# Kernel tuning notes

Measured on AMD Instinct MI355X. Metric: run time of the kernel, lower is better.

## Reference

```python
import jax, jax.numpy as jnp
import numpy as np
from jax import lax

L = 15      # time_conv_size
STRIDE = 2


def setup_inputs() -> dict:
    key = jax.random.key(0)
    k1, k2, k3 = jax.random.split(key, 3)
    x = jax.random.normal(k1, (8, 4096, 64), dtype=jnp.float32)
    w1 = jax.random.normal(k2, (L,), dtype=jnp.float32)
    w2 = jax.random.normal(k3, (L,), dtype=jnp.float32)
    return {"x": x, "w1": w1, "w2": w2}


def reference(x, w1, w2):
    # x: [B, T, C]; w1, w2: [L]
    B, T, C = x.shape
    p = L // 2
    # --- weighted local mean: mu[b,t,c] = sum_k w1[k] * x_pad[b,t+k,c] ---
    x_pad = jnp.pad(x, ((0, 0), (p, p), (0, 0)))
    mu = sum(w1[k] * x_pad[:, k:k + T, :] for k in range(L))  # [B,T,C]
    # --- centered diagonal bilinear (covariance) pooling ---
    xc_pad = jnp.pad(x - mu, ((0, 0), (p, p), (0, 0)))  # [B, T+2p, C]
    # strided window indices: I = ceil(T/STRIDE) windows of length L
    starts = jnp.arange(0, T, STRIDE)                   # [I]
    idx = starts[:, None] + jnp.arange(L)[None, :]      # [I, L]
    win = xc_pad[:, idx, :]                             # [B, I, L, C]
    sigma = jnp.einsum('bilc,l,bild->bicd', win, w2, win)
    I = starts.shape[0]
    sigma = sigma.reshape(B, I, C * C)
    mu_s = mu[:, ::STRIDE, :]                           # [B, I, C]
    out = jnp.concatenate([mu_s, sigma], axis=-1)       # [B, I, C + C*C]
    # K.l2_normalize over last axis (epsilon=1e-12)
    denom = lax.rsqrt(jnp.maximum(jnp.sum(out * out, axis=-1, keepdims=True), 1e-12))
    return out * denom
```

## Files before the change

kernel.cpp:

```cpp
#include <hip/hip_runtime.h>

#define Tdim 4096
#define Bdim 8
#define Cdim 64
#define Ldim 15
#define Idim 2048
#define OUTW 4160

__global__ __launch_bounds__(256) void cbp_kernel(const float* __restrict__ x,
                                                  const float* __restrict__ w1,
                                                  const float* __restrict__ w2,
                                                  float* __restrict__ out) {
    __shared__ float xbuf[29][64];
    __shared__ float xcs[15][64];
    __shared__ float mus[64];
    __shared__ float w1s[16], w2s[16];
    __shared__ float red[4];
    __shared__ float scale_s;

    const int tid = threadIdx.x;
    const int blk = blockIdx.x;
    const int b = blk >> 11;
    const int i = blk & (Idim - 1);
    const int s = i << 1;

    if (tid < Ldim) { w1s[tid] = w1[tid]; w2s[tid] = w2[tid]; }

    const float* xb = x + (size_t)b * Tdim * Cdim;
    for (int v = tid; v < 29 * 16; v += 256) {
        const int r = v >> 4;
        const int c4 = (v & 15) << 2;
        const int t = s - 14 + r;
        float4 val = make_float4(0.f, 0.f, 0.f, 0.f);
        if (t >= 0 && t < Tdim) val = *(const float4*)(xb + (size_t)t * Cdim + c4);
        *(float4*)(&xbuf[r][c4]) = val;
    }
    __syncthreads();

    if (tid < 240) {
        const int l = tid >> 4;
        const int c4 = (tid & 15) << 2;
        const int t = s - 7 + l;
        float4 m = make_float4(0.f, 0.f, 0.f, 0.f);
#pragma unroll
        for (int k = 0; k < Ldim; ++k) {
            const float w = w1s[k];
            const float4 xv = *(const float4*)(&xbuf[l + k][c4]);
            m.x = fmaf(w, xv.x, m.x);
            m.y = fmaf(w, xv.y, m.y);
            m.z = fmaf(w, xv.z, m.z);
            m.w = fmaf(w, xv.w, m.w);
        }
        const float4 xv = *(const float4*)(&xbuf[l + 7][c4]);
        float4 xc;
        if (t >= 0 && t < Tdim) {
            xc = make_float4(xv.x - m.x, xv.y - m.y, xv.z - m.z, xv.w - m.w);
        } else {
            xc = make_float4(0.f, 0.f, 0.f, 0.f);
        }
        *(float4*)(&xcs[l][c4]) = xc;
        if (l == 7) *(float4*)(&mus[c4]) = m;
    }
    __syncthreads();

    const int q  = tid >> 4;
    const int d0 = (tid & 15) << 2;
    float acc[4][4];
#pragma unroll
    for (int jj = 0; jj < 4; ++jj)
#pragma unroll
        for (int dd = 0; dd < 4; ++dd) acc[jj][dd] = 0.f;

#pragma unroll
    for (int l = 0; l < Ldim; ++l) {
        const float4 xd = *(const float4*)(&xcs[l][d0]);
        const float w = w2s[l];
#pragma unroll
        for (int jj = 0; jj < 4; ++jj) {
            const float a = w * xcs[l][jj * 16 + q];
            acc[jj][0] = fmaf(a, xd.x, acc[jj][0]);
            acc[jj][1] = fmaf(a, xd.y, acc[jj][1]);
            acc[jj][2] = fmaf(a, xd.z, acc[jj][2]);
            acc[jj][3] = fmaf(a, xd.w, acc[jj][3]);
        }
    }

    float local = 0.f;
#pragma unroll
    for (int jj = 0; jj < 4; ++jj)
#pragma unroll
        for (int dd = 0; dd < 4; ++dd) local = fmaf(acc[jj][dd], acc[jj][dd], local);
    if (tid < Cdim) local = fmaf(mus[tid], mus[tid], local);

#pragma unroll
    for (int off = 32; off; off >>= 1) local += __shfl_down(local, off, 64);
    if ((tid & 63) == 0) red[tid >> 6] = local;
    __syncthreads();
    if (tid == 0) {
        const float ss = red[0] + red[1] + red[2] + red[3];
        scale_s = rsqrtf(fmaxf(ss, 1e-12f));
    }
    __syncthreads();
    const float sc = scale_s;

    float* orow = out + (size_t)blk * OUTW;
    if (tid < 16) {
        float4 m4 = *(const float4*)(&mus[tid << 2]);
        m4.x *= sc; m4.y *= sc; m4.z *= sc; m4.w *= sc;
        *(float4*)(orow + (tid << 2)) = m4;
    }
    float* osig = orow + Cdim;
#pragma unroll
    for (int jj = 0; jj < 4; ++jj) {
        const float4 v = make_float4(acc[jj][0] * sc, acc[jj][1] * sc,
                                     acc[jj][2] * sc, acc[jj][3] * sc);
        *(float4*)(osig + jj * 1024 + (tid << 2)) = v;
    }
}

extern "C" void kernel_launch(void* const* d_in, const int* in_sizes, int n_in,
                              void* d_out, int out_size, void* d_ws, size_t ws_size,
                              hipStream_t stream) {
    const float* x  = (const float*)d_in[0];
    const float* w1 = (const float*)d_in[1];
    const float* w2 = (const float*)d_in[2];
    float* out = (float*)d_out;
    cbp_kernel<<<dim3(Bdim * Idim), dim3(256), 0, stream>>>(x, w1, w2, out);
}
```

Baseline: 309.2 us.

## Process four output windows per block sharing loaded and centered rows

Each block now computes four consecutive strided windows instead of one, so overlapping input rows are loaded and centered once and the mean is computed for 21 rows rather than 15 per window. Each thread now holds a 4x4 c-by-d tile per window (64 accumulators), so every shared-memory read feeds more FMAs. Weights are read straight from global memory instead of being staged in shared memory, and launch bounds request 4 blocks per CU. The cost is much higher register pressure and four times fewer blocks.

```diff
diff --git a/kernel.cpp b/kernel.cpp
--- a/kernel.cpp
+++ b/kernel.cpp
@@ -6,115 +6,147 @@
 #define Ldim 15
 #define Idim 2048
 #define OUTW 4160
+#define G    4
+#define RX   (2*G + 27)
+#define RXC  (2*G + 13)
 
-__global__ __launch_bounds__(256) void cbp_kernel(const float* __restrict__ x,
-                                                  const float* __restrict__ w1,
-                                                  const float* __restrict__ w2,
-                                                  float* __restrict__ out) {
-    __shared__ float xbuf[29][64];
-    __shared__ float xcs[15][64];
-    __shared__ float mus[64];
-    __shared__ float w1s[16], w2s[16];
-    __shared__ float red[4];
-    __shared__ float scale_s;
+__global__ __launch_bounds__(256, 4) void cbp_kernel(const float* __restrict__ x,
+                                                     const float* __restrict__ w1,
+                                                     const float* __restrict__ w2,
+                                                     float* __restrict__ out) {
+    __shared__ float xbuf[RX][64];
+    __shared__ float xcs[RXC][64];
+    __shared__ float mus[G][64];
+    __shared__ float red[4][G];
+    __shared__ float scale_s[G];
 
     const int tid = threadIdx.x;
     const int blk = blockIdx.x;
-    const int b = blk >> 11;
-    const int i = blk & (Idim - 1);
-    const int s = i << 1;
+    const int b  = blk >> 9;
+    const int i0 = (blk & 511) << 2;
+    const int s0 = i0 << 1;
 
-    if (tid < Ldim) { w1s[tid] = w1[tid]; w2s[tid] = w2[tid]; }
-
-    const float* xb = x + (size_t)b * Tdim * Cdim;
-    for (int v = tid; v < 29 * 16; v += 256) {
-        const int r = v >> 4;
+    const float* xb = x + (size_t)b * (Tdim * Cdim);
+    for (int v = tid; v < RX * 16; v += 256) {
+        const int r  = v >> 4;
         const int c4 = (v & 15) << 2;
-        const int t = s - 14 + r;
+        const int t  = s0 - 14 + r;
         float4 val = make_float4(0.f, 0.f, 0.f, 0.f);
         if (t >= 0 && t < Tdim) val = *(const float4*)(xb + (size_t)t * Cdim + c4);
         *(float4*)(&xbuf[r][c4]) = val;
     }
     __syncthreads();
 
-    if (tid < 240) {
-        const int l = tid >> 4;
-        const int c4 = (tid & 15) << 2;
-        const int t = s - 7 + l;
+    for (int v = tid; v < RXC * 16; v += 256) {
+        const int j  = v >> 4;
+        const int c4 = (v & 15) << 2;
+        const int t  = s0 - 7 + j;
         float4 m = make_float4(0.f, 0.f, 0.f, 0.f);
 #pragma unroll
         for (int k = 0; k < Ldim; ++k) {
-            const float w = w1s[k];
-            const float4 xv = *(const float4*)(&xbuf[l + k][c4]);
+            const float w = w1[k];
+            const float4 xv = *(const float4*)(&xbuf[j + k][c4]);
             m.x = fmaf(w, xv.x, m.x);
             m.y = fmaf(w, xv.y, m.y);
             m.z = fmaf(w, xv.z, m.z);
             m.w = fmaf(w, xv.w, m.w);
         }
-        const float4 xv = *(const float4*)(&xbuf[l + 7][c4]);
-        float4 xc;
-        if (t >= 0 && t < Tdim) {
+        const float4 xv = *(const float4*)(&xbuf[j + 7][c4]);
+        float4 xc = make_float4(0.f, 0.f, 0.f, 0.f);
+        if (t >= 0 && t < Tdim)
             xc = make_float4(xv.x - m.x, xv.y - m.y, xv.z - m.z, xv.w - m.w);
-        } else {
-            xc = make_float4(0.f, 0.f, 0.f, 0.f);
-        }
-        *(float4*)(&xcs[l][c4]) = xc;
-        if (l == 7) *(float4*)(&mus[c4]) = m;
+        *(float4*)(&xcs[j][c4]) = xc;
+        if (j >= 7 && j <= 13 && ((j - 7) & 1) == 0)
+            *(float4*)(&mus[(j - 7) >> 1][c4]) = m;
     }
     __syncthreads();
 
-    const int q  = tid >> 4;
+    const int c0 = (tid >> 4) << 2;
     const int d0 = (tid & 15) << 2;
-    float acc[4][4];
+    float acc[G][4][4];
 #pragma unroll
-    for (int jj = 0; jj < 4; ++jj)
+    for (int g = 0; g < G; ++g)
 #pragma unroll
-        for (int dd = 0; dd < 4; ++dd) acc[jj][dd] = 0.f;
+        for (int cc = 0; cc < 4; ++cc)
+#pragma unroll
+            for (int dd = 0; dd < 4; ++dd) acc[g][cc][dd] = 0.f;
 
 #pragma unroll
-    for (int l = 0; l < Ldim; ++l) {
-        const float4 xd = *(const float4*)(&xcs[l][d0]);
-        const float w = w2s[l];
+    for (int r = 0; r < RXC; ++r) {
+        const float4 xd = *(const float4*)(&xcs[r][d0]);
+        const float4 xc = *(const float4*)(&xcs[r][c0]);
 #pragma unroll
-        for (int jj = 0; jj < 4; ++jj) {
-            const float a = w * xcs[l][jj * 16 + q];
-            acc[jj][0] = fmaf(a, xd.x, acc[jj][0]);
-            acc[jj][1] = fmaf(a, xd.y, acc[jj][1]);
-            acc[jj][2] = fmaf(a, xd.z, acc[jj][2]);
-            acc[jj][3] = fmaf(a, xd.w, acc[jj][3]);
+        for (int g = 0; g < G; ++g) {
+            const int l = r - 2 * g;
+            if (l >= 0 && l < Ldim) {
+                const float w  = w2[l];
+                const float a0 = w * xc.x, a1 = w * xc.y, a2 = w * xc.z, a3 = w * xc.w;
+                acc[g][0][0] = fmaf(a0, xd.x, acc[g][0][0]);
+                acc[g][0][1] = fmaf(a0, xd.y, acc[g][0][1]);
+                acc[g][0][2] = fmaf(a0, xd.z, acc[g][0][2]);
+                acc[g][0][3] = fmaf(a0, xd.w, acc[g][0][3]);
+                acc[g][1][0] = fmaf(a1, xd.x, acc[g][1][0]);
+                acc[g][1][1] = fmaf(a1, xd.y, acc[g][1][1]);
+                acc[g][1][2] = fmaf(a1, xd.z, acc[g][1][2]);
+                acc[g][1][3] = fmaf(a1, xd.w, acc[g][1][3]);
+                acc[g][2][0] = fmaf(a2, xd.x, acc[g][2][0]);
+                acc[g][2][1] = fmaf(a2, xd.y, acc[g][2][1]);
+                acc[g][2][2] = fmaf(a2, xd.z, acc[g][2][2]);
+                acc[g][2][3] = fmaf(a2, xd.w, acc[g][2][3]);
+                acc[g][3][0] = fmaf(a3, xd.x, acc[g][3][0]);
+                acc[g][3][1] = fmaf(a3, xd.y, acc[g][3][1]);
+                acc[g][3][2] = fmaf(a3, xd.z, acc[g][3][2]);
+                acc[g][3][3] = fmaf(a3, xd.w, acc[g][3][3]);
+            }
         }
     }
 
-    float local = 0.f;
+    float local[G];
 #pragma unroll
-    for (int jj = 0; jj < 4; ++jj)
+    for (int g = 0; g < G; ++g) {
+        float s = 0.f;
 #pragma unroll
-        for (int dd = 0; dd < 4; ++dd) local = fmaf(acc[jj][dd], acc[jj][dd], local);
-    if (tid < Cdim) local = fmaf(mus[tid], mus[tid], local);
+        for (int cc = 0; cc < 4; ++cc)
+#pragma unroll
+            for (int dd = 0; dd < 4; ++dd) s = fmaf(acc[g][cc][dd], acc[g][cc][dd], s);
+        local[g] = s;
+    }
+    if (tid < Cdim) {
+#pragma unroll
+        for (int g = 0; g < G; ++g) local[g] = fmaf(mus[g][tid], mus[g][tid], local[g]);
+    }
+#pragma unroll
+    for (int off = 32; off; off >>= 1)
+#pragma unroll
+        for (int g = 0; g < G; ++g) local[g] += __shfl_down(local[g], off, 64);
+    if ((tid & 63) == 0) {
+        const int w = tid >> 6;
+#pragma unroll
+        for (int g = 0; g < G; ++g) red[w][g] = local[g];
+    }
+    __syncthreads();
+    if (tid < G) {
+        const float ss = red[0][tid] + red[1][tid] + red[2][tid] + red[3][tid];
+        scale_s[tid] = rsqrtf(fmaxf(ss, 1e-12f));
+    }
+    __syncthreads();
 
 #pragma unroll
-    for (int off = 32; off; off >>= 1) local += __shfl_down(local, off, 64);
-    if ((tid & 63) == 0) red[tid >> 6] = local;
-    __syncthreads();
-    if (tid == 0) {
-        const float ss = red[0] + red[1] + red[2] + red[3];
-        scale_s = rsqrtf(fmaxf(ss, 1e-12f));
-    }
-    __syncthreads();
-    const float sc = scale_s;
-
-    float* orow = out + (size_t)blk * OUTW;
-    if (tid < 16) {
-        float4 m4 = *(const float4*)(&mus[tid << 2]);
-        m4.x *= sc; m4.y *= sc; m4.z *= sc; m4.w *= sc;
-        *(float4*)(orow + (tid << 2)) = m4;
-    }
-    float* osig = orow + Cdim;
+    for (int g = 0; g < G; ++g) {
+        const float sc = scale_s[g];
+        float* orow = out + (size_t)(b * Idim + i0 + g) * OUTW;
+        if (tid < 16) {
+            float4 m4 = *(const float4*)(&mus[g][tid << 2]);
+            m4.x *= sc; m4.y *= sc; m4.z *= sc; m4.w *= sc;
+            *(float4*)(orow + (tid << 2)) = m4;
+        }
+        float* osig = orow + Cdim;
 #pragma unroll
-    for (int jj = 0; jj < 4; ++jj) {
-        const float4 v = make_float4(acc[jj][0] * sc, acc[jj][1] * sc,
-                                     acc[jj][2] * sc, acc[jj][3] * sc);
-        *(float4*)(osig + jj * 1024 + (tid << 2)) = v;
+        for (int cc = 0; cc < 4; ++cc) {
+            const float4 v = make_float4(acc[g][cc][0] * sc, acc[g][cc][1] * sc,
+                                         acc[g][cc][2] * sc, acc[g][cc][3] * sc);
+            *(float4*)(osig + (c0 + cc) * Cdim + d0) = v;
+        }
     }
 }
 
@@ -125,5 +157,5 @@
     const float* w1 = (const float*)d_in[1];
     const float* w2 = (const float*)d_in[2];
     float* out = (float*)d_out;
-    cbp_kernel<<<dim3(Bdim * Idim), dim3(256), 0, stream>>>(x, w1, w2, out);
+    cbp_kernel<<<dim3(Bdim * (Idim / G)), dim3(256), 0, stream>>>(x, w1, w2, out);
 }
```

After: 289.3 us. 1.07x faster.
